# Kernel tuning notes

Measured on AMD Instinct MI355X. Metric: run time of the kernel, lower is better.

Reference implementation:

```python
import jax, jax.numpy as jnp
import numpy as np

D = 1024
H = 16
HEAD_DIM = D // H

def setup_inputs() -> dict:
    key = jax.random.key(0)
    ks = jax.random.split(key, 5)
    B, T = 2, 2048
    scale = 0.02
    x = jax.random.normal(ks[0], (B, T, D), dtype=jnp.float32)
    W_kqv = jax.random.normal(ks[1], (D, 3 * D), dtype=jnp.float32) * scale
    b_kqv = jnp.zeros((3 * D,), dtype=jnp.float32)
    W_proj = jax.random.normal(ks[2], (D, D), dtype=jnp.float32) * scale
    b_proj = jnp.zeros((D,), dtype=jnp.float32)
    return {"x": x, "W_kqv": W_kqv, "b_kqv": b_kqv, "W_proj": W_proj, "b_proj": b_proj}

def reference(x, W_kqv, b_kqv, W_proj, b_proj):
    B, T, d = x.shape
    qkv = x @ W_kqv + b_kqv  # [B,T,3d]
    q, k, v = jnp.split(qkv, 3, axis=-1)
    # [B, h, T, head_dim]
    def heads(t):
        return t.reshape(B, T, H, HEAD_DIM).transpose(0, 2, 1, 3)
    q, k, v = heads(q), heads(k), heads(v)
    scores = jnp.einsum("bhqd,bhkd->bhqk", q, k) / jnp.sqrt(jnp.float32(HEAD_DIM))
    causal = jnp.tril(jnp.ones((T, T), dtype=bool))  # True = keep
    scores = jnp.where(causal[None, None], scores, -jnp.inf)
    attn = jax.nn.softmax(scores, axis=-1)
    out = jnp.einsum("bhqk,bhkd->bhqd", attn, v)
    out = out.transpose(0, 2, 1, 3).reshape(B, T, d)
    return out @ W_proj + b_proj
```

## Files before the change

### kernel.cpp

```cpp
#include <hip/hip_runtime.h>
#include <hip/hip_bf16.h>
#include <cstdint>

typedef __bf16 bf16_t;
typedef __bf16 bf16x8 __attribute__((ext_vector_type(8)));
typedef __bf16 bf16x4 __attribute__((ext_vector_type(4)));
typedef float  f32x4  __attribute__((ext_vector_type(4)));

static constexpr int Bb = 2;
static constexpr int Tt = 2048;
static constexpr int Dd = 1024;
static constexpr int Hh = 16;
static constexpr int HD = 64;

#define QSCALE 0.18033688011112042f
#define SSHIFT 16.0f

__device__ __forceinline__ void async_copy16(const bf16_t* gsrc, bf16_t* ldst) {
    __builtin_amdgcn_global_load_lds(
        (const __attribute__((address_space(1))) unsigned int*)gsrc,
        (__attribute__((address_space(3))) unsigned int*)ldst, 16, 0, 0);
}

__global__ __launch_bounds__(256) void prep_kernel(
    const float* __restrict__ x, bf16_t* __restrict__ x_bf,
    const float* __restrict__ Wk, bf16_t* __restrict__ wkqvt,
    const float* __restrict__ Wp, bf16_t* __restrict__ wprojt) {
    __shared__ bf16_t tile[64][72];
    int bid = blockIdx.x;
    int t = threadIdx.x;
    if (bid < 2048) {
        int i = (bid * 256 + t) * 8;
        float4 v0 = *(const float4*)(x + i);
        float4 v1 = *(const float4*)(x + i + 4);
        bf16x8 o;
        o[0] = (bf16_t)v0.x; o[1] = (bf16_t)v0.y; o[2] = (bf16_t)v0.z; o[3] = (bf16_t)v0.w;
        o[4] = (bf16_t)v1.x; o[5] = (bf16_t)v1.y; o[6] = (bf16_t)v1.z; o[7] = (bf16_t)v1.w;
        *(bf16x8*)(x_bf + i) = o;
        return;
    }
    const float* in; bf16_t* out; int R, C, tr, tc;
    if (bid < 2816) {
        int id = bid - 2048;
        R = Dd; C = 3 * Dd;
        tc = (id % 48) * 64; tr = (id / 48) * 64;
        in = Wk; out = wkqvt;
    } else {
        int id = bid - 2816;
        R = Dd; C = Dd;
        tc = (id & 15) * 64; tr = (id >> 4) * 64;
        in = Wp; out = wprojt;
    }
    int r = t >> 4;
    int c4 = (t & 15) * 4;
#pragma unroll
    for (int rr = 0; rr < 4; ++rr) {
        int row = r + rr * 16;
        float4 v = *(const float4*)(in + (size_t)(tr + row) * C + tc + c4);
        tile[c4 + 0][row] = (bf16_t)v.x;
        tile[c4 + 1][row] = (bf16_t)v.y;
        tile[c4 + 2][row] = (bf16_t)v.z;
        tile[c4 + 3][row] = (bf16_t)v.w;
    }
    __syncthreads();
#pragma unroll
    for (int rr = 0; rr < 4; ++rr) {
        int oc = r + rr * 16;
        bf16x4 o;
        o[0] = tile[oc][c4 + 0];
        o[1] = tile[oc][c4 + 1];
        o[2] = tile[oc][c4 + 2];
        o[3] = tile[oc][c4 + 3];
        *(bf16x4*)(out + (size_t)(tc + oc) * R + tr + c4) = o;
    }
}

template <int MODE, int NT>
__global__ __launch_bounds__(256) void gemm_bt(
    const bf16_t* __restrict__ A, const bf16_t* __restrict__ Bt,
    const float* __restrict__ bias, float* __restrict__ Cout,
    bf16_t* __restrict__ qb_, bf16_t* __restrict__ kb_, bf16_t* __restrict__ vb_,
    int M, int N, int K) {
    constexpr int NFRAG = NT / 32;
    __shared__ bf16_t As[128 * 64];
    __shared__ bf16_t Bs[NT * 64];
    int t = threadIdx.x;
    int wave = t >> 6, lane = t & 63;
    int l15 = lane & 15, quad = lane >> 4;
    int wm = wave & 1, wn = wave >> 1;
    int m0 = blockIdx.y * 128, n0 = blockIdx.x * NT;

    f32x4 acc[4][NFRAG];
#pragma unroll
    for (int mi = 0; mi < 4; ++mi)
#pragma unroll
        for (int ni = 0; ni < NFRAG; ++ni) acc[mi][ni] = (f32x4){0.f, 0.f, 0.f, 0.f};

    int kx = l15 & 7;

    for (int kk = 0; kk < K; kk += 64) {
        __syncthreads();
#pragma unroll
        for (int j = 0; j < 4; ++j) {
            int cid = j * 256 + t;
            int row = cid >> 3, sub = (cid & 7) ^ (row & 7);
            async_copy16(A + (size_t)(m0 + row) * K + kk + sub * 8, &As[cid * 8]);
        }
#pragma unroll
        for (int j = 0; j < NT / 32; ++j) {
            int cid = j * 256 + t;
            int row = cid >> 3, sub = (cid & 7) ^ (row & 7);
            async_copy16(Bt + (size_t)(n0 + row) * K + kk + sub * 8, &Bs[cid * 8]);
        }
        __syncthreads();
#pragma unroll
        for (int kb = 0; kb < 2; ++kb) {
            bf16x8 af[4], bf[NFRAG];
#pragma unroll
            for (int mi = 0; mi < 4; ++mi) {
                int r = wm * 64 + mi * 16 + l15;
                af[mi] = *(const bf16x8*)(&As[r * 64 + ((kb * 4 + quad) ^ kx) * 8]);
            }
#pragma unroll
            for (int ni = 0; ni < NFRAG; ++ni) {
                int r = wn * (NT / 2) + ni * 16 + l15;
                bf[ni] = *(const bf16x8*)(&Bs[r * 64 + ((kb * 4 + quad) ^ kx) * 8]);
            }
#pragma unroll
            for (int mi = 0; mi < 4; ++mi)
#pragma unroll
                for (int ni = 0; ni < NFRAG; ++ni)
                    acc[mi][ni] = __builtin_amdgcn_mfma_f32_16x16x32_bf16(bf[ni], af[mi], acc[mi][ni], 0, 0, 0);
        }
    }

    int sec = n0 >> 10;
    if (MODE == 1 && sec == 2) {
#pragma unroll
        for (int ni = 0; ni < NFRAG; ++ni) {
            int n = n0 + wn * (NT / 2) + ni * 16 + quad * 4;
            int hh = (n >> 6) & 15, dd0 = n & 63;
            f32x4 bv4 = *(const f32x4*)(bias + n);
#pragma unroll
            for (int mi = 0; mi < 4; ++mi) {
                int row = m0 + wm * 64 + mi * 16 + l15;
                int bb = row >> 11, tt = row & (Tt - 1);
#pragma unroll
                for (int r = 0; r < 4; ++r)
                    vb_[((size_t)(bb * Hh + hh) * HD + dd0 + r) * Tt + tt] =
                        (bf16_t)(acc[mi][ni][r] + bv4[r]);
            }
        }
        return;
    }
    if (MODE == 1) {
        float sc = (sec == 0) ? QSCALE : 1.0f;
        bf16_t* dst = (sec == 0) ? qb_ : kb_;
#pragma unroll
        for (int ni = 0; ni < NFRAG; ++ni) {
            int n = n0 + wn * (NT / 2) + ni * 16 + quad * 4;
            int hh = (n >> 6) & 15, dd0 = n & 63;
            f32x4 bv4 = *(const f32x4*)(bias + n);
#pragma unroll
            for (int mi = 0; mi < 4; ++mi) {
                int row = m0 + wm * 64 + mi * 16 + l15;
                int bb = row >> 11, tt = row & (Tt - 1);
                bf16x4 pv;
#pragma unroll
                for (int r = 0; r < 4; ++r) pv[r] = (bf16_t)((acc[mi][ni][r] + bv4[r]) * sc);
                *(bf16x4*)(dst + ((size_t)(bb * Hh + hh) * Tt + tt) * HD + dd0) = pv;
            }
        }
        return;
    }
#pragma unroll
    for (int mi = 0; mi < 4; ++mi) {
        int m = m0 + wm * 64 + mi * 16 + l15;
#pragma unroll
        for (int ni = 0; ni < NFRAG; ++ni) {
            int n = n0 + wn * (NT / 2) + ni * 16 + quad * 4;
            f32x4 bv4 = *(const f32x4*)(bias + n);
            f32x4 ov = acc[mi][ni] + bv4;
            *(f32x4*)(Cout + (size_t)m * N + n) = ov;
        }
    }
}

__global__ __launch_bounds__(256, 4) void attn_kernel(
    const bf16_t* __restrict__ qb, const bf16_t* __restrict__ kb,
    const bf16_t* __restrict__ vb, bf16_t* __restrict__ ab) {
    __shared__ bf16_t Ks[64][72];
    __shared__ bf16_t Vs[64][72];
    int t = threadIdx.x;
    int wave = t >> 6, lane = t & 63;
    int l15 = lane & 15, quad = lane >> 4;
    int bh = blockIdx.x;
    int qt = 31 - (int)blockIdx.y;
    int b = bh >> 4, h = bh & 15;
    int qbase = qt * 64 + wave * 16;
    int q = qbase + l15;
    const bf16_t* qptr = qb + (size_t)bh * Tt * HD;
    const bf16_t* kptr = kb + (size_t)bh * Tt * HD;
    const bf16_t* vptr = vb + (size_t)bh * HD * Tt;

    bf16x8 qf[2];
    qf[0] = *(const bf16x8*)(qptr + (size_t)q * HD + quad * 8);
    qf[1] = *(const bf16x8*)(qptr + (size_t)q * HD + 32 + quad * 8);

    f32x4 o[4];
#pragma unroll
    for (int g = 0; g < 4; ++g) o[g] = (f32x4){0.f, 0.f, 0.f, 0.f};
    float lrow = 0.f;

    int srow = t >> 2;
    int scol = (t & 3) * 16;
    int c0 = (t & 3) * 2, c1 = c0 + 1;
    int vb0 = ((c0 >> 2) * 32) + ((c0 & 1) * 16) + (((c0 >> 1) & 1) * 4);
    int vb1 = ((c1 >> 2) * 32) + ((c1 & 1) * 16) + (((c1 >> 1) & 1) * 4);

    int nkt = qt + 1;

    bf16x8 kr0, kr1, vr0, vr1;
    {
        const bf16_t* kg = kptr + (size_t)srow * HD + scol;
        kr0 = *(const bf16x8*)(kg);
        kr1 = *(const bf16x8*)(kg + 8);
        const bf16_t* vg = vptr + (size_t)srow * Tt + scol;
        vr0 = *(const bf16x8*)(vg);
        vr1 = *(const bf16x8*)(vg + 8);
    }

    const f32x4 sinit = (f32x4){-SSHIFT, -SSHIFT, -SSHIFT, -SSHIFT};

    for (int it = 0; it < nkt; ++it) {
        int kt0 = it * 64;
        __syncthreads();
        *(bf16x8*)(&Ks[srow][scol])     = kr0;
        *(bf16x8*)(&Ks[srow][scol + 8]) = kr1;
        *(bf16x4*)(&Vs[srow][vb0])     = __builtin_shufflevector(vr0, vr0, 0, 1, 2, 3);
        *(bf16x4*)(&Vs[srow][vb0 + 8]) = __builtin_shufflevector(vr0, vr0, 4, 5, 6, 7);
        *(bf16x4*)(&Vs[srow][vb1])     = __builtin_shufflevector(vr1, vr1, 0, 1, 2, 3);
        *(bf16x4*)(&Vs[srow][vb1 + 8]) = __builtin_shufflevector(vr1, vr1, 4, 5, 6, 7);
        __syncthreads();
        if (it + 1 < nkt) {
            int kt = (it + 1) * 64;
            const bf16_t* kg = kptr + (size_t)(kt + srow) * HD + scol;
            kr0 = *(const bf16x8*)(kg);
            kr1 = *(const bf16x8*)(kg + 8);
            const bf16_t* vg = vptr + (size_t)srow * Tt + kt + scol;
            vr0 = *(const bf16x8*)(vg);
            vr1 = *(const bf16x8*)(vg + 8);
        }

        f32x4 s[4];
#pragma unroll
        for (int g = 0; g < 4; ++g) {
            s[g] = sinit;
            bf16x8 kf0 = *(const bf16x8*)(&Ks[g * 16 + l15][quad * 8]);
            bf16x8 kf1 = *(const bf16x8*)(&Ks[g * 16 + l15][32 + quad * 8]);
            s[g] = __builtin_amdgcn_mfma_f32_16x16x32_bf16(kf0, qf[0], s[g], 0, 0, 0);
            s[g] = __builtin_amdgcn_mfma_f32_16x16x32_bf16(kf1, qf[1], s[g], 0, 0, 0);
        }

        if (kt0 + 63 > qbase) {
#pragma unroll
            for (int g = 0; g < 4; ++g)
#pragma unroll
                for (int r = 0; r < 4; ++r) {
                    int k_abs = kt0 + g * 16 + quad * 4 + r;
                    s[g][r] = (k_abs > q) ? -1e30f : s[g][r];
                }
        }

        bf16x4 pk[4];
#pragma unroll
        for (int g = 0; g < 4; ++g) {
            float p0 = exp2f(s[g][0]);
            float p1 = exp2f(s[g][1]);
            float p2 = exp2f(s[g][2]);
            float p3 = exp2f(s[g][3]);
            lrow += (p0 + p1) + (p2 + p3);
            pk[g][0] = (bf16_t)p0; pk[g][1] = (bf16_t)p1;
            pk[g][2] = (bf16_t)p2; pk[g][3] = (bf16_t)p3;
        }

#pragma unroll
        for (int kc = 0; kc < 2; ++kc) {
            bf16x8 pf = __builtin_shufflevector(pk[kc * 2], pk[kc * 2 + 1],
                                                0, 1, 2, 3, 4, 5, 6, 7);
#pragma unroll
            for (int g = 0; g < 4; ++g) {
                bf16x8 vf = *(const bf16x8*)(&Vs[g * 16 + l15][kc * 32 + quad * 8]);
                o[g] = __builtin_amdgcn_mfma_f32_16x16x32_bf16(vf, pf, o[g], 0, 0, 0);
            }
        }
    }

    lrow += __shfl_xor(lrow, 16);
    lrow += __shfl_xor(lrow, 32);
    float inv = 1.0f / lrow;
    size_t obase = ((size_t)b * Tt + q) * Dd + h * 64;
#pragma unroll
    for (int g = 0; g < 4; ++g) {
        bf16x4 ov;
#pragma unroll
        for (int r = 0; r < 4; ++r) ov[r] = (bf16_t)(o[g][r] * inv);
        *(bf16x4*)(ab + obase + g * 16 + quad * 4) = ov;
    }
}

extern "C" void kernel_launch(void* const* d_in, const int* in_sizes, int n_in,
                              void* d_out, int out_size, void* d_ws, size_t ws_size,
                              hipStream_t stream) {
    const float* x      = (const float*)d_in[0];
    const float* W_kqv  = (const float*)d_in[1];
    const float* b_kqv  = (const float*)d_in[2];
    const float* W_proj = (const float*)d_in[3];
    const float* b_proj = (const float*)d_in[4];
    float* out = (float*)d_out;
    char* ws = (char*)d_ws;
    const size_t MB = 1ull << 20;
    bf16_t* x_bf   = (bf16_t*)(ws + 0 * MB);
    bf16_t* wkqvt  = (bf16_t*)(ws + 8 * MB);
    bf16_t* wprojt = (bf16_t*)(ws + 14 * MB);
    bf16_t* qb     = (bf16_t*)(ws + 16 * MB);
    bf16_t* kb     = (bf16_t*)(ws + 24 * MB);
    bf16_t* vb     = (bf16_t*)(ws + 32 * MB);
    bf16_t* ab     = (bf16_t*)(ws + 40 * MB);

    prep_kernel<<<3072, 256, 0, stream>>>(x, x_bf, W_kqv, wkqvt, W_proj, wprojt);
    gemm_bt<1, 64><<<dim3(3 * Dd / 64, Bb * Tt / 128), 256, 0, stream>>>(
        x_bf, wkqvt, b_kqv, nullptr, qb, kb, vb, Bb * Tt, 3 * Dd, Dd);
    attn_kernel<<<dim3(Bb * Hh, 32), 256, 0, stream>>>(qb, kb, vb, ab);
    gemm_bt<0, 64><<<dim3(Dd / 64, Bb * Tt / 128), 256, 0, stream>>>(
        ab, wprojt, b_proj, out, nullptr, nullptr, nullptr, Bb * Tt, Dd, Dd);
}
```

Before: 177.6 us.

## Fuse x fp32-to-bf16 conversion into QKV GEMM, widen attention K tiles, shrink proj tile

Drops the separate x conversion from the prep kernel; the QKV GEMM now loads fp32 x directly and converts to bf16 on the way into LDS, skipping one global round trip. The attention kernel stages 128 keys per barrier pair instead of 64, processing two 64-key subtiles per iteration to halve synchronisation. The output projection GEMM uses NT=32 to launch more blocks. The fused fp32 load is synchronous rather than async-to-LDS and reads twice the bytes per tile for every N block, so the A operand is re-read as fp32 across 48 column blocks.

```diff
diff --git a/kernel.cpp b/kernel.cpp
--- a/kernel.cpp
+++ b/kernel.cpp
@@ -23,30 +23,18 @@
 }
 
 __global__ __launch_bounds__(256) void prep_kernel(
-    const float* __restrict__ x, bf16_t* __restrict__ x_bf,
     const float* __restrict__ Wk, bf16_t* __restrict__ wkqvt,
     const float* __restrict__ Wp, bf16_t* __restrict__ wprojt) {
     __shared__ bf16_t tile[64][72];
     int bid = blockIdx.x;
     int t = threadIdx.x;
-    if (bid < 2048) {
-        int i = (bid * 256 + t) * 8;
-        float4 v0 = *(const float4*)(x + i);
-        float4 v1 = *(const float4*)(x + i + 4);
-        bf16x8 o;
-        o[0] = (bf16_t)v0.x; o[1] = (bf16_t)v0.y; o[2] = (bf16_t)v0.z; o[3] = (bf16_t)v0.w;
-        o[4] = (bf16_t)v1.x; o[5] = (bf16_t)v1.y; o[6] = (bf16_t)v1.z; o[7] = (bf16_t)v1.w;
-        *(bf16x8*)(x_bf + i) = o;
-        return;
-    }
     const float* in; bf16_t* out; int R, C, tr, tc;
-    if (bid < 2816) {
-        int id = bid - 2048;
+    if (bid < 768) {
         R = Dd; C = 3 * Dd;
-        tc = (id % 48) * 64; tr = (id / 48) * 64;
+        tc = (bid % 48) * 64; tr = (bid / 48) * 64;
         in = Wk; out = wkqvt;
     } else {
-        int id = bid - 2816;
+        int id = bid - 768;
         R = Dd; C = Dd;
         tc = (id & 15) * 64; tr = (id >> 4) * 64;
         in = Wp; out = wprojt;
@@ -75,9 +63,9 @@
     }
 }
 
-template <int MODE, int NT>
+template <int MODE, int NT, bool AF32>
 __global__ __launch_bounds__(256) void gemm_bt(
-    const bf16_t* __restrict__ A, const bf16_t* __restrict__ Bt,
+    const void* __restrict__ Av, const bf16_t* __restrict__ Bt,
     const float* __restrict__ bias, float* __restrict__ Cout,
     bf16_t* __restrict__ qb_, bf16_t* __restrict__ kb_, bf16_t* __restrict__ vb_,
     int M, int N, int K) {
@@ -100,11 +88,30 @@
 
     for (int kk = 0; kk < K; kk += 64) {
         __syncthreads();
-#pragma unroll
-        for (int j = 0; j < 4; ++j) {
-            int cid = j * 256 + t;
-            int row = cid >> 3, sub = (cid & 7) ^ (row & 7);
-            async_copy16(A + (size_t)(m0 + row) * K + kk + sub * 8, &As[cid * 8]);
+        if (AF32) {
+            const float* Af = (const float*)Av;
+#pragma unroll
+            for (int j = 0; j < 4; ++j) {
+                int cid = j * 256 + t;
+                int row = cid >> 3, sub = (cid & 7) ^ (row & 7);
+                const float* ag = Af + (size_t)(m0 + row) * K + kk + sub * 8;
+                float4 v0 = *(const float4*)(ag);
+                float4 v1 = *(const float4*)(ag + 4);
+                bf16x8 o;
+                o[0] = (bf16_t)v0.x; o[1] = (bf16_t)v0.y;
+                o[2] = (bf16_t)v0.z; o[3] = (bf16_t)v0.w;
+                o[4] = (bf16_t)v1.x; o[5] = (bf16_t)v1.y;
+                o[6] = (bf16_t)v1.z; o[7] = (bf16_t)v1.w;
+                *(bf16x8*)(&As[cid * 8]) = o;
+            }
+        } else {
+            const bf16_t* Ab = (const bf16_t*)Av;
+#pragma unroll
+            for (int j = 0; j < 4; ++j) {
+                int cid = j * 256 + t;
+                int row = cid >> 3, sub = (cid & 7) ^ (row & 7);
+                async_copy16(Ab + (size_t)(m0 + row) * K + kk + sub * 8, &As[cid * 8]);
+            }
         }
 #pragma unroll
         for (int j = 0; j < NT / 32; ++j) {
@@ -189,8 +196,8 @@
 __global__ __launch_bounds__(256, 4) void attn_kernel(
     const bf16_t* __restrict__ qb, const bf16_t* __restrict__ kb,
     const bf16_t* __restrict__ vb, bf16_t* __restrict__ ab) {
-    __shared__ bf16_t Ks[64][72];
-    __shared__ bf16_t Vs[64][72];
+    __shared__ bf16_t Ks[128][72];
+    __shared__ bf16_t Vs[64][136];
     int t = threadIdx.x;
     int wave = t >> 6, lane = t & 63;
     int l15 = lane & 15, quad = lane >> 4;
@@ -212,86 +219,88 @@
     for (int g = 0; g < 4; ++g) o[g] = (f32x4){0.f, 0.f, 0.f, 0.f};
     float lrow = 0.f;
 
-    int srow = t >> 2;
-    int scol = (t & 3) * 16;
-    int c0 = (t & 3) * 2, c1 = c0 + 1;
-    int vb0 = ((c0 >> 2) * 32) + ((c0 & 1) * 16) + (((c0 >> 1) & 1) * 4);
-    int vb1 = ((c1 >> 2) * 32) + ((c1 & 1) * 16) + (((c1 >> 1) & 1) * 4);
-
-    int nkt = qt + 1;
-
-    bf16x8 kr0, kr1, vr0, vr1;
-    {
-        const bf16_t* kg = kptr + (size_t)srow * HD + scol;
-        kr0 = *(const bf16x8*)(kg);
-        kr1 = *(const bf16x8*)(kg + 8);
-        const bf16_t* vg = vptr + (size_t)srow * Tt + scol;
-        vr0 = *(const bf16x8*)(vg);
-        vr1 = *(const bf16x8*)(vg + 8);
+    int nR = (qt >> 1) + 1;
+    bf16x8 kpr[4], vpr[4];
+#pragma unroll
+    for (int j = 0; j < 4; ++j) {
+        int cid = j * 256 + t;
+        kpr[j] = *(const bf16x8*)(kptr + (size_t)(cid >> 3) * HD + (cid & 7) * 8);
+        vpr[j] = *(const bf16x8*)(vptr + (size_t)(cid >> 4) * Tt + (cid & 15) * 8);
     }
 
     const f32x4 sinit = (f32x4){-SSHIFT, -SSHIFT, -SSHIFT, -SSHIFT};
 
-    for (int it = 0; it < nkt; ++it) {
-        int kt0 = it * 64;
+    for (int it2 = 0; it2 < nR; ++it2) {
         __syncthreads();
-        *(bf16x8*)(&Ks[srow][scol])     = kr0;
-        *(bf16x8*)(&Ks[srow][scol + 8]) = kr1;
-        *(bf16x4*)(&Vs[srow][vb0])     = __builtin_shufflevector(vr0, vr0, 0, 1, 2, 3);
-        *(bf16x4*)(&Vs[srow][vb0 + 8]) = __builtin_shufflevector(vr0, vr0, 4, 5, 6, 7);
-        *(bf16x4*)(&Vs[srow][vb1])     = __builtin_shufflevector(vr1, vr1, 0, 1, 2, 3);
-        *(bf16x4*)(&Vs[srow][vb1 + 8]) = __builtin_shufflevector(vr1, vr1, 4, 5, 6, 7);
+#pragma unroll
+        for (int j = 0; j < 4; ++j) {
+            int cid = j * 256 + t;
+            *(bf16x8*)(&Ks[cid >> 3][(cid & 7) * 8]) = kpr[j];
+            int vd = cid >> 4, kc = cid & 15;
+            int pb = (kc >> 2) * 32 + (kc & 1) * 16 + ((kc >> 1) & 1) * 4;
+            *(bf16x4*)(&Vs[vd][pb])     = __builtin_shufflevector(vpr[j], vpr[j], 0, 1, 2, 3);
+            *(bf16x4*)(&Vs[vd][pb + 8]) = __builtin_shufflevector(vpr[j], vpr[j], 4, 5, 6, 7);
+        }
         __syncthreads();
-        if (it + 1 < nkt) {
-            int kt = (it + 1) * 64;
-            const bf16_t* kg = kptr + (size_t)(kt + srow) * HD + scol;
-            kr0 = *(const bf16x8*)(kg);
-            kr1 = *(const bf16x8*)(kg + 8);
-            const bf16_t* vg = vptr + (size_t)srow * Tt + kt + scol;
-            vr0 = *(const bf16x8*)(vg);
-            vr1 = *(const bf16x8*)(vg + 8);
-        }
-
-        f32x4 s[4];
-#pragma unroll
-        for (int g = 0; g < 4; ++g) {
-            s[g] = sinit;
-            bf16x8 kf0 = *(const bf16x8*)(&Ks[g * 16 + l15][quad * 8]);
-            bf16x8 kf1 = *(const bf16x8*)(&Ks[g * 16 + l15][32 + quad * 8]);
-            s[g] = __builtin_amdgcn_mfma_f32_16x16x32_bf16(kf0, qf[0], s[g], 0, 0, 0);
-            s[g] = __builtin_amdgcn_mfma_f32_16x16x32_bf16(kf1, qf[1], s[g], 0, 0, 0);
-        }
-
-        if (kt0 + 63 > qbase) {
-#pragma unroll
-            for (int g = 0; g < 4; ++g)
-#pragma unroll
-                for (int r = 0; r < 4; ++r) {
-                    int k_abs = kt0 + g * 16 + quad * 4 + r;
-                    s[g][r] = (k_abs > q) ? -1e30f : s[g][r];
+        if (it2 + 1 < nR) {
+            int kt = (it2 + 1) * 128;
+#pragma unroll
+            for (int j = 0; j < 4; ++j) {
+                int cid = j * 256 + t;
+                kpr[j] = *(const bf16x8*)(kptr + (size_t)(kt + (cid >> 3)) * HD + (cid & 7) * 8);
+                vpr[j] = *(const bf16x8*)(vptr + (size_t)(cid >> 4) * Tt + kt + (cid & 15) * 8);
+            }
+        }
+
+#pragma unroll
+        for (int sub = 0; sub < 2; ++sub) {
+            int tidx = it2 * 2 + sub;
+            if (tidx <= qt) {
+                int kt0 = tidx * 64;
+
+                f32x4 s[4];
+#pragma unroll
+                for (int g = 0; g < 4; ++g) {
+                    s[g] = sinit;
+                    int krow = sub * 64 + g * 16 + l15;
+                    bf16x8 kf0 = *(const bf16x8*)(&Ks[krow][quad * 8]);
+                    bf16x8 kf1 = *(const bf16x8*)(&Ks[krow][32 + quad * 8]);
+                    s[g] = __builtin_amdgcn_mfma_f32_16x16x32_bf16(kf0, qf[0], s[g], 0, 0, 0);
+                    s[g] = __builtin_amdgcn_mfma_f32_16x16x32_bf16(kf1, qf[1], s[g], 0, 0, 0);
                 }
-        }
-
-        bf16x4 pk[4];
-#pragma unroll
-        for (int g = 0; g < 4; ++g) {
-            float p0 = exp2f(s[g][0]);
-            float p1 = exp2f(s[g][1]);
-            float p2 = exp2f(s[g][2]);
-            float p3 = exp2f(s[g][3]);
-            lrow += (p0 + p1) + (p2 + p3);
-            pk[g][0] = (bf16_t)p0; pk[g][1] = (bf16_t)p1;
-            pk[g][2] = (bf16_t)p2; pk[g][3] = (bf16_t)p3;
-        }
-
-#pragma unroll
-        for (int kc = 0; kc < 2; ++kc) {
-            bf16x8 pf = __builtin_shufflevector(pk[kc * 2], pk[kc * 2 + 1],
-                                                0, 1, 2, 3, 4, 5, 6, 7);
-#pragma unroll
-            for (int g = 0; g < 4; ++g) {
-                bf16x8 vf = *(const bf16x8*)(&Vs[g * 16 + l15][kc * 32 + quad * 8]);
-                o[g] = __builtin_amdgcn_mfma_f32_16x16x32_bf16(vf, pf, o[g], 0, 0, 0);
+
+                if (kt0 + 63 > qbase) {
+#pragma unroll
+                    for (int g = 0; g < 4; ++g)
+#pragma unroll
+                        for (int r = 0; r < 4; ++r) {
+                            int k_abs = kt0 + g * 16 + quad * 4 + r;
+                            s[g][r] = (k_abs > q) ? -1e30f : s[g][r];
+                        }
+                }
+
+                bf16x4 pk[4];
+#pragma unroll
+                for (int g = 0; g < 4; ++g) {
+                    float p0 = exp2f(s[g][0]);
+                    float p1 = exp2f(s[g][1]);
+                    float p2 = exp2f(s[g][2]);
+                    float p3 = exp2f(s[g][3]);
+                    lrow += (p0 + p1) + (p2 + p3);
+                    pk[g][0] = (bf16_t)p0; pk[g][1] = (bf16_t)p1;
+                    pk[g][2] = (bf16_t)p2; pk[g][3] = (bf16_t)p3;
+                }
+
+#pragma unroll
+                for (int kc = 0; kc < 2; ++kc) {
+                    bf16x8 pf = __builtin_shufflevector(pk[kc * 2], pk[kc * 2 + 1],
+                                                        0, 1, 2, 3, 4, 5, 6, 7);
+#pragma unroll
+                    for (int g = 0; g < 4; ++g) {
+                        bf16x8 vf = *(const bf16x8*)(&Vs[g * 16 + l15][sub * 64 + kc * 32 + quad * 8]);
+                        o[g] = __builtin_amdgcn_mfma_f32_16x16x32_bf16(vf, pf, o[g], 0, 0, 0);
+                    }
+                }
             }
         }
     }
@@ -320,7 +329,6 @@
     float* out = (float*)d_out;
     char* ws = (char*)d_ws;
     const size_t MB = 1ull << 20;
-    bf16_t* x_bf   = (bf16_t*)(ws + 0 * MB);
     bf16_t* wkqvt  = (bf16_t*)(ws + 8 * MB);
     bf16_t* wprojt = (bf16_t*)(ws + 14 * MB);
     bf16_t* qb     = (bf16_t*)(ws + 16 * MB);
@@ -328,10 +336,10 @@
     bf16_t* vb     = (bf16_t*)(ws + 32 * MB);
     bf16_t* ab     = (bf16_t*)(ws + 40 * MB);
 
-    prep_kernel<<<3072, 256, 0, stream>>>(x, x_bf, W_kqv, wkqvt, W_proj, wprojt);
-    gemm_bt<1, 64><<<dim3(3 * Dd / 64, Bb * Tt / 128), 256, 0, stream>>>(
-        x_bf, wkqvt, b_kqv, nullptr, qb, kb, vb, Bb * Tt, 3 * Dd, Dd);
+    prep_kernel<<<1024, 256, 0, stream>>>(W_kqv, wkqvt, W_proj, wprojt);
+    gemm_bt<1, 64, true><<<dim3(3 * Dd / 64, Bb * Tt / 128), 256, 0, stream>>>(
+        (const void*)x, wkqvt, b_kqv, nullptr, qb, kb, vb, Bb * Tt, 3 * Dd, Dd);
     attn_kernel<<<dim3(Bb * Hh, 32), 256, 0, stream>>>(qb, kb, vb, ab);
-    gemm_bt<0, 64><<<dim3(Dd / 64, Bb * Tt / 128), 256, 0, stream>>>(
-        ab, wprojt, b_proj, out, nullptr, nullptr, nullptr, Bb * Tt, Dd, Dd);
-}
+    gemm_bt<0, 32, false><<<dim3(Dd / 32, Bb * Tt / 128), 256, 0, stream>>>(
+        (const void*)ab, wprojt, b_proj, out, nullptr, nullptr, nullptr, Bb * Tt, Dd, Dd);
+}
```

Result: slower. 194.8 us (+9.7%).
